# Optimization experiments

Measured on AMD Instinct MI355X. Metric: run time of the kernel, lower is better.

The kernel has to match this reference:

```python
import jax, jax.numpy as jnp
import numpy as np

B, S, H, I, E, TOP_K = 2, 1024, 1024, 2048, 8, 2


def setup_inputs() -> dict:
    key = jax.random.key(0)
    ks = jax.random.split(key, 5)
    return {
        "hidden_states": jax.random.normal(ks[0], (B, S, H), jnp.float32),
        # torch Linear weights are (out, in)
        "router_w": jax.random.normal(ks[1], (E, H), jnp.float32) * 0.02,
        "w1": jax.random.normal(ks[2], (E, I, H), jnp.float32) * 0.02,
        "v": jax.random.normal(ks[3], (E, I, H), jnp.float32) * 0.02,
        "w2": jax.random.normal(ks[4], (E, H, I), jnp.float32) * 0.02,
    }


def _moe(x, router_w, w1, v, w2):
    # x: [T, H] flattened tokens
    T = x.shape[0]
    n_exp = router_w.shape[0]
    logits = x @ router_w.T                                    # [T, E]
    probs = jax.nn.softmax(logits.astype(jnp.float32), axis=-1)
    top_p, top_i = jax.lax.top_k(probs, TOP_K)                 # [T, K]
    top_p = top_p / top_p.sum(axis=-1, keepdims=True)
    top_p = top_p.astype(x.dtype)
    # dense gate matrix [T, E]; zero for unselected experts -> identical math
    # to the torch gather / index_add combine
    gates = jnp.zeros((T, n_exp), x.dtype).at[
        jnp.arange(T)[:, None], top_i].set(top_p)
    out = jnp.zeros_like(x)
    for e in range(n_exp):  # small fixed expert loop keeps peak memory low
        h = jax.nn.gelu(x @ w1[e].T, approximate=False) * (x @ v[e].T)  # [T, I]
        out = out + gates[:, e:e + 1] * (h @ w2[e].T)                   # [T, H]
    return out, logits


def reference(hidden_states, router_w, w1, v, w2):
    b, s, h = hidden_states.shape
    out, logits = _moe(hidden_states.reshape(-1, h), router_w, w1, v, w2)
    return out.reshape(b, s, h), logits
```

## Files before the change

kernel.cpp:

```cpp
#include <hip/hip_runtime.h>
#include <math.h>

#define T 2048
#define HD 1024
#define ID 2048
#define NE 8
#define CSTRIDE 32

typedef short bf16x8 __attribute__((ext_vector_type(8)));
typedef float f32x4 __attribute__((ext_vector_type(4)));
typedef unsigned short u16x4 __attribute__((ext_vector_type(4)));

__device__ __forceinline__ unsigned short f2bf(float f) {
  union { float f; unsigned u; } v; v.f = f;
  unsigned r = v.u + 0x7FFFu + ((v.u >> 16) & 1u);
  return (unsigned short)(r >> 16);
}

__device__ __forceinline__ void cast_chunk16(const float* __restrict__ s,
                                             unsigned short* __restrict__ d,
                                             size_t base) {
  size_t o = base + (size_t)threadIdx.x * 4;
#pragma unroll
  for (int k = 0; k < 4; k++) {
    float4 f = *(const float4*)(s + o + k * 1024);
    u16x4 h;
    h[0] = f2bf(f.x); h[1] = f2bf(f.y); h[2] = f2bf(f.z); h[3] = f2bf(f.w);
    *(u16x4*)(d + o + k * 1024) = h;
  }
}

__device__ __forceinline__ void glds16(const unsigned short* g, unsigned short* l) {
  __builtin_amdgcn_global_load_lds(
      (const __attribute__((address_space(1))) unsigned int*)(g),
      (__attribute__((address_space(3))) unsigned int*)(l), 16, 0, 0);
}

__global__ __launch_bounds__(256) void prep_kernel(
    const float* __restrict__ x, const float* __restrict__ rw,
    const float* __restrict__ w1, const float* __restrict__ v,
    unsigned short* __restrict__ xb, unsigned short* __restrict__ w1b,
    unsigned short* __restrict__ vb, float* __restrict__ logits_out,
    int* __restrict__ pair_rowid, float* __restrict__ pair_gate,
    int* __restrict__ counts) {
  int bx = blockIdx.x;
  if (bx >= 768) {
    int cid = bx - 768;
    const float* s = (cid < 4096) ? w1 : v;
    unsigned short* d = (cid < 4096) ? w1b : vb;
    cast_chunk16(s, d, (size_t)(cid & 4095) * 4096);
    return;
  }
  if (bx >= 256) {
    cast_chunk16(x, xb, (size_t)(bx - 256) * 4096);
    return;
  }
  __shared__ int s_e[16];
  __shared__ int s_rid[16];
  __shared__ float s_gt[16];
  int tid = threadIdx.x;
  int wid = tid >> 6, lane = tid & 63;
  for (int tk = 0; tk < 2; ++tk) {
    int t = bx * 8 + wid * 2 + tk;
    float acc[NE];
#pragma unroll
    for (int e = 0; e < NE; e++) acc[e] = 0.f;
    const float* xrow = x + (size_t)t * HD;
#pragma unroll 2
    for (int j = 0; j < HD; j += 64) {
      float xv = xrow[j + lane];
#pragma unroll
      for (int e = 0; e < NE; e++) acc[e] += xv * rw[e * HD + j + lane];
    }
#pragma unroll
    for (int e = 0; e < NE; e++)
      for (int off = 32; off > 0; off >>= 1) acc[e] += __shfl_xor(acc[e], off, 64);
    if (lane == 0) {
#pragma unroll
      for (int e = 0; e < NE; e++) logits_out[t * NE + e] = acc[e];
      int e0 = 0;
#pragma unroll
      for (int e = 1; e < NE; e++) if (acc[e] > acc[e0]) e0 = e;
      int e1 = (e0 == 0) ? 1 : 0;
#pragma unroll
      for (int e = 0; e < NE; e++)
        if (e != e0 && e != e1 && acc[e] > acc[e1]) e1 = e;
      float b = __expf(acc[e1] - acc[e0]);
      float g0 = 1.f / (1.f + b);
      float g1 = 1.f - g0;
      int slot = (wid * 2 + tk) * 2;
      s_e[slot] = e0; s_rid[slot] = t * 2;     s_gt[slot] = g0;
      s_e[slot + 1] = e1; s_rid[slot + 1] = t * 2 + 1; s_gt[slot + 1] = g1;
    }
  }
  __syncthreads();
  if (tid < NE) {
    int cnt = 0;
#pragma unroll
    for (int k = 0; k < 16; k++) if (s_e[k] == tid) cnt++;
    if (cnt) {
      int base = atomicAdd(&counts[tid * CSTRIDE], cnt);
      int p = 0;
      for (int k = 0; k < 16; k++)
        if (s_e[k] == tid) {
          pair_rowid[tid * T + base + p] = s_rid[k];
          pair_gate[tid * T + base + p] = s_gt[k];
          p++;
        }
    }
  }
}

__global__ __launch_bounds__(256) void gemm1_kernel(
    const unsigned short* __restrict__ xb, const unsigned short* __restrict__ w1b,
    const unsigned short* __restrict__ vb, unsigned short* __restrict__ hb,
    const float* __restrict__ w2, unsigned short* __restrict__ w2b,
    const int* __restrict__ pair_rowid, const int* __restrict__ counts) {
  if (blockIdx.x >= 32) {
    int cid = (blockIdx.x - 32) + 32 * (blockIdx.y + 16 * blockIdx.z);
    cast_chunk16(w2, w2b, (size_t)cid * 4096);
    return;
  }
  int e = blockIdx.z;
  int cnt = counts[e * CSTRIDE];
  int row0 = blockIdx.y * 128;
  if (row0 >= cnt) return;
  __shared__ unsigned short As[128 * 64];
  __shared__ unsigned short B1s[64 * 64];
  __shared__ unsigned short B2s[64 * 64];
  __shared__ int rids[128];
  int tid = threadIdx.x;
  if (tid < 128) {
    int idx = row0 + tid; if (idx > cnt - 1) idx = cnt - 1;
    rids[tid] = pair_rowid[e * T + idx];
  }
  __syncthreads();
  int lane = tid & 63, wid = tid >> 6;
  int wr = wid >> 1, wc = wid & 1;
  int col0 = blockIdx.x * 64;
  int gr = lane >> 3, gc = lane & 7;
  const unsigned short *aA[4], *aB1[2], *aB2[2];
#pragma unroll
  for (int c = 0; c < 4; c++) {
    int row = (c * 4 + wid) * 8 + gr;
    int tok = rids[row] >> 1;
    aA[c] = xb + (size_t)tok * HD + ((gc ^ (row & 7)) * 8);
  }
#pragma unroll
  for (int c = 0; c < 2; c++) {
    int row = (c * 4 + wid) * 8 + gr;
    int kswz = ((gc ^ (row & 7)) * 8);
    aB1[c] = w1b + ((size_t)(e * ID + col0 + row)) * HD + kswz;
    aB2[c] = vb  + ((size_t)(e * ID + col0 + row)) * HD + kswz;
  }
  f32x4 acc1[4][2] = {};
  f32x4 acc3[4][2] = {};
  int mrow = lane & 15, kq = lane >> 4;
  int swzm = mrow & 7;
  for (int kt = 0; kt < HD; kt += 64) {
#pragma unroll
    for (int c = 0; c < 4; c++)
      glds16(aA[c] + kt, &As[(c * 4 + wid) * 512]);
#pragma unroll
    for (int c = 0; c < 2; c++) {
      glds16(aB1[c] + kt, &B1s[(c * 4 + wid) * 512]);
      glds16(aB2[c] + kt, &B2s[(c * 4 + wid) * 512]);
    }
    __syncthreads();
#pragma unroll
    for (int kk = 0; kk < 2; kk++) {
      int g = kk * 4 + kq;
      int ko = ((g ^ swzm) * 8);
      bf16x8 a[4], b1[2], b2[2];
#pragma unroll
      for (int mi = 0; mi < 4; mi++)
        a[mi] = *(const bf16x8*)&As[(wr * 64 + mi * 16 + mrow) * 64 + ko];
#pragma unroll
      for (int ni = 0; ni < 2; ni++) {
        b1[ni] = *(const bf16x8*)&B1s[(wc * 32 + ni * 16 + mrow) * 64 + ko];
        b2[ni] = *(const bf16x8*)&B2s[(wc * 32 + ni * 16 + mrow) * 64 + ko];
      }
#pragma unroll
      for (int mi = 0; mi < 4; mi++)
#pragma unroll
        for (int ni = 0; ni < 2; ni++) {
          acc1[mi][ni] = __builtin_amdgcn_mfma_f32_16x16x32_bf16(a[mi], b1[ni], acc1[mi][ni], 0, 0, 0);
          acc3[mi][ni] = __builtin_amdgcn_mfma_f32_16x16x32_bf16(a[mi], b2[ni], acc3[mi][ni], 0, 0, 0);
        }
    }
    __syncthreads();
  }
  int dcol = lane & 15, drow4 = (lane >> 4) * 4;
#pragma unroll
  for (int mi = 0; mi < 4; mi++)
#pragma unroll
    for (int ni = 0; ni < 2; ni++)
#pragma unroll
      for (int r = 0; r < 4; r++) {
        int lr = wr * 64 + mi * 16 + drow4 + r;
        if (row0 + lr < cnt) {
          float g1v = acc1[mi][ni][r];
          float g3v = acc3[mi][ni][r];
          float hval = 0.5f * g1v * (1.f + erff(g1v * 0.70710678118654752f)) * g3v;
          int rowid = rids[lr];
          hb[(size_t)rowid * ID + col0 + wc * 32 + ni * 16 + dcol] = f2bf(hval);
        }
      }
}

__global__ __launch_bounds__(256) void gemm2_kernel(
    const unsigned short* __restrict__ hb, const unsigned short* __restrict__ w2b,
    float* __restrict__ yb, const int* __restrict__ pair_rowid,
    const float* __restrict__ pair_gate, const int* __restrict__ counts) {
  int e = blockIdx.z;
  int cnt = counts[e * CSTRIDE];
  int row0 = blockIdx.y * 64;
  if (row0 >= cnt) return;
  __shared__ unsigned short As[64 * 64];
  __shared__ unsigned short Bs[64 * 64];
  __shared__ int rids[64];
  __shared__ float gts[64];
  int tid = threadIdx.x;
  if (tid < 64) {
    int idx = row0 + tid; if (idx > cnt - 1) idx = cnt - 1;
    rids[tid] = pair_rowid[e * T + idx];
    gts[tid] = pair_gate[e * T + idx];
  }
  __syncthreads();
  int lane = tid & 63, wid = tid >> 6;
  int wr = wid >> 1, wc = wid & 1;
  int col0 = blockIdx.x * 64;
  int gr = lane >> 3, gc = lane & 7;
  const unsigned short *aA[2], *aB[2];
#pragma unroll
  for (int c = 0; c < 2; c++) {
    int row = (c * 4 + wid) * 8 + gr;
    int kswz = ((gc ^ (row & 7)) * 8);
    aA[c] = hb  + (size_t)rids[row] * ID + kswz;
    aB[c] = w2b + ((size_t)(e * HD + col0 + row)) * ID + kswz;
  }
  f32x4 acc[2][2] = {};
  int mrow = lane & 15, kq = lane >> 4;
  int swzm = mrow & 7;
  for (int kt = 0; kt < ID; kt += 64) {
#pragma unroll
    for (int c = 0; c < 2; c++) {
      glds16(aA[c] + kt, &As[(c * 4 + wid) * 512]);
      glds16(aB[c] + kt, &Bs[(c * 4 + wid) * 512]);
    }
    __syncthreads();
#pragma unroll
    for (int kk = 0; kk < 2; kk++) {
      int g = kk * 4 + kq;
      int ko = ((g ^ swzm) * 8);
      bf16x8 a[2], b[2];
#pragma unroll
      for (int mi = 0; mi < 2; mi++)
        a[mi] = *(const bf16x8*)&As[(wr * 32 + mi * 16 + mrow) * 64 + ko];
#pragma unroll
      for (int ni = 0; ni < 2; ni++)
        b[ni] = *(const bf16x8*)&Bs[(wc * 32 + ni * 16 + mrow) * 64 + ko];
#pragma unroll
      for (int mi = 0; mi < 2; mi++)
#pragma unroll
        for (int ni = 0; ni < 2; ni++)
          acc[mi][ni] = __builtin_amdgcn_mfma_f32_16x16x32_bf16(a[mi], b[ni], acc[mi][ni], 0, 0, 0);
    }
    __syncthreads();
  }
  int dcol = lane & 15, drow4 = (lane >> 4) * 4;
#pragma unroll
  for (int mi = 0; mi < 2; mi++)
#pragma unroll
    for (int ni = 0; ni < 2; ni++)
#pragma unroll
      for (int r = 0; r < 4; r++) {
        int lr = wr * 32 + mi * 16 + drow4 + r;
        if (row0 + lr < cnt) {
          float val = gts[lr] * acc[mi][ni][r];
          yb[(size_t)rids[lr] * HD + col0 + wc * 32 + ni * 16 + dcol] = val;
        }
      }
}

__global__ __launch_bounds__(256) void combine_kernel(
    const float* __restrict__ yb, float* __restrict__ out) {
  size_t t = blockIdx.x;
  int c = threadIdx.x * 4;
  float4 a = *(const float4*)(yb + (t * 2) * HD + c);
  float4 b = *(const float4*)(yb + (t * 2 + 1) * HD + c);
  float4 o;
  o.x = a.x + b.x; o.y = a.y + b.y; o.z = a.z + b.z; o.w = a.w + b.w;
  *(float4*)(out + t * HD + c) = o;
}

extern "C" void kernel_launch(void* const* d_in, const int* in_sizes, int n_in,
                              void* d_out, int out_size, void* d_ws, size_t ws_size,
                              hipStream_t stream) {
  const float* x  = (const float*)d_in[0];
  const float* rw = (const float*)d_in[1];
  const float* w1 = (const float*)d_in[2];
  const float* v  = (const float*)d_in[3];
  const float* w2 = (const float*)d_in[4];
  float* out = (float*)d_out;
  float* logits_out = out + (size_t)T * HD;

  char* ws = (char*)d_ws;
  unsigned short* xb  = (unsigned short*)(ws);
  unsigned short* hb  = (unsigned short*)(ws + (4u << 20));
  unsigned short* w1b = (unsigned short*)(ws + (20u << 20));
  unsigned short* vb  = (unsigned short*)(ws + (52u << 20));
  unsigned short* w2b = (unsigned short*)(ws + (84u << 20));
  float* yb           = (float*)(ws + (20u << 20));
  int*   pair_rowid   = (int*)  (ws + (116u << 20));
  float* pair_gate    = (float*)(ws + (116u << 20) + 65536);
  int*   counts       = (int*)  (ws + (116u << 20) + 131072);

  hipMemsetAsync(counts, 0, NE * CSTRIDE * sizeof(int), stream);

  prep_kernel<<<8960, 256, 0, stream>>>(x, rw, w1, v, xb, w1b, vb,
                                        logits_out, pair_rowid, pair_gate,
                                        counts);
  gemm1_kernel<<<dim3(ID / 64 + 32, T / 128, NE), 256, 0, stream>>>(
      xb, w1b, vb, hb, w2, w2b, pair_rowid, counts);
  gemm2_kernel<<<dim3(HD / 64, T / 64, NE), 256, 0, stream>>>(
      hb, w2b, yb, pair_rowid, pair_gate, counts);
  combine_kernel<<<T, 256, 0, stream>>>(yb, out);
}
```

Before: 327.7 us.

## Fuse fp32-to-bf16 weight casts into double-buffered expert GEMM loads

```diff
diff --git a/kernel.cpp b/kernel.cpp
--- a/kernel.cpp
+++ b/kernel.cpp
@@ -10,11 +10,19 @@
 typedef short bf16x8 __attribute__((ext_vector_type(8)));
 typedef float f32x4 __attribute__((ext_vector_type(4)));
 typedef unsigned short u16x4 __attribute__((ext_vector_type(4)));
+typedef unsigned short u16x8 __attribute__((ext_vector_type(8)));
 
 __device__ __forceinline__ unsigned short f2bf(float f) {
   union { float f; unsigned u; } v; v.f = f;
   unsigned r = v.u + 0x7FFFu + ((v.u >> 16) & 1u);
   return (unsigned short)(r >> 16);
+}
+
+__device__ __forceinline__ u16x8 cvt8(float4 a, float4 b) {
+  u16x8 o;
+  o[0] = f2bf(a.x); o[1] = f2bf(a.y); o[2] = f2bf(a.z); o[3] = f2bf(a.w);
+  o[4] = f2bf(b.x); o[5] = f2bf(b.y); o[6] = f2bf(b.z); o[7] = f2bf(b.w);
+  return o;
 }
 
 __device__ __forceinline__ void cast_chunk16(const float* __restrict__ s,
@@ -38,19 +46,10 @@
 
 __global__ __launch_bounds__(256) void prep_kernel(
     const float* __restrict__ x, const float* __restrict__ rw,
-    const float* __restrict__ w1, const float* __restrict__ v,
-    unsigned short* __restrict__ xb, unsigned short* __restrict__ w1b,
-    unsigned short* __restrict__ vb, float* __restrict__ logits_out,
+    unsigned short* __restrict__ xb, float* __restrict__ logits_out,
     int* __restrict__ pair_rowid, float* __restrict__ pair_gate,
     int* __restrict__ counts) {
   int bx = blockIdx.x;
-  if (bx >= 768) {
-    int cid = bx - 768;
-    const float* s = (cid < 4096) ? w1 : v;
-    unsigned short* d = (cid < 4096) ? w1b : vb;
-    cast_chunk16(s, d, (size_t)(cid & 4095) * 4096);
-    return;
-  }
   if (bx >= 256) {
     cast_chunk16(x, xb, (size_t)(bx - 256) * 4096);
     return;
@@ -112,61 +111,62 @@
 }
 
 __global__ __launch_bounds__(256) void gemm1_kernel(
-    const unsigned short* __restrict__ xb, const unsigned short* __restrict__ w1b,
-    const unsigned short* __restrict__ vb, unsigned short* __restrict__ hb,
-    const float* __restrict__ w2, unsigned short* __restrict__ w2b,
+    const unsigned short* __restrict__ xb, const float* __restrict__ w1,
+    const float* __restrict__ v, unsigned short* __restrict__ hb,
     const int* __restrict__ pair_rowid, const int* __restrict__ counts) {
-  if (blockIdx.x >= 32) {
-    int cid = (blockIdx.x - 32) + 32 * (blockIdx.y + 16 * blockIdx.z);
-    cast_chunk16(w2, w2b, (size_t)cid * 4096);
-    return;
-  }
   int e = blockIdx.z;
   int cnt = counts[e * CSTRIDE];
   int row0 = blockIdx.y * 128;
   if (row0 >= cnt) return;
-  __shared__ unsigned short As[128 * 64];
-  __shared__ unsigned short B1s[64 * 64];
-  __shared__ unsigned short B2s[64 * 64];
-  __shared__ int rids[128];
+  __shared__ unsigned short As[2][128 * 64];
+  __shared__ unsigned short B1s[2][64 * 64];
+  __shared__ unsigned short B2s[2][64 * 64];
   int tid = threadIdx.x;
-  if (tid < 128) {
-    int idx = row0 + tid; if (idx > cnt - 1) idx = cnt - 1;
-    rids[tid] = pair_rowid[e * T + idx];
-  }
-  __syncthreads();
   int lane = tid & 63, wid = tid >> 6;
   int wr = wid >> 1, wc = wid & 1;
   int col0 = blockIdx.x * 64;
   int gr = lane >> 3, gc = lane & 7;
-  const unsigned short *aA[4], *aB1[2], *aB2[2];
+  const unsigned short *aA[4];
+  const float *aB1[2], *aB2[2];
 #pragma unroll
   for (int c = 0; c < 4; c++) {
     int row = (c * 4 + wid) * 8 + gr;
-    int tok = rids[row] >> 1;
+    int idx = row0 + row; if (idx > cnt - 1) idx = cnt - 1;
+    int tok = pair_rowid[e * T + idx] >> 1;
     aA[c] = xb + (size_t)tok * HD + ((gc ^ (row & 7)) * 8);
   }
 #pragma unroll
   for (int c = 0; c < 2; c++) {
     int row = (c * 4 + wid) * 8 + gr;
     int kswz = ((gc ^ (row & 7)) * 8);
-    aB1[c] = w1b + ((size_t)(e * ID + col0 + row)) * HD + kswz;
-    aB2[c] = vb  + ((size_t)(e * ID + col0 + row)) * HD + kswz;
+    aB1[c] = w1 + ((size_t)(e * ID + col0 + row)) * HD + kswz;
+    aB2[c] = v  + ((size_t)(e * ID + col0 + row)) * HD + kswz;
   }
   f32x4 acc1[4][2] = {};
   f32x4 acc3[4][2] = {};
   int mrow = lane & 15, kq = lane >> 4;
   int swzm = mrow & 7;
-  for (int kt = 0; kt < HD; kt += 64) {
-#pragma unroll
-    for (int c = 0; c < 4; c++)
-      glds16(aA[c] + kt, &As[(c * 4 + wid) * 512]);
+  float4 rb1[2][2], rb2[2][2];
+
+  auto issue = [&](int buf, int kt) {
+#pragma unroll
+    for (int c = 0; c < 4; c++) glds16(aA[c] + kt, &As[buf][(c * 4 + wid) * 512]);
 #pragma unroll
     for (int c = 0; c < 2; c++) {
-      glds16(aB1[c] + kt, &B1s[(c * 4 + wid) * 512]);
-      glds16(aB2[c] + kt, &B2s[(c * 4 + wid) * 512]);
-    }
-    __syncthreads();
+      rb1[c][0] = *(const float4*)(aB1[c] + kt);
+      rb1[c][1] = *(const float4*)(aB1[c] + kt + 4);
+      rb2[c][0] = *(const float4*)(aB2[c] + kt);
+      rb2[c][1] = *(const float4*)(aB2[c] + kt + 4);
+    }
+  };
+  auto commitB = [&](int buf) {
+#pragma unroll
+    for (int c = 0; c < 2; c++) {
+      *(u16x8*)&B1s[buf][(c * 4 + wid) * 512 + lane * 8] = cvt8(rb1[c][0], rb1[c][1]);
+      *(u16x8*)&B2s[buf][(c * 4 + wid) * 512 + lane * 8] = cvt8(rb2[c][0], rb2[c][1]);
+    }
+  };
+  auto compute = [&](int buf) {
 #pragma unroll
     for (int kk = 0; kk < 2; kk++) {
       int g = kk * 4 + kq;
@@ -174,11 +174,11 @@
       bf16x8 a[4], b1[2], b2[2];
 #pragma unroll
       for (int mi = 0; mi < 4; mi++)
-        a[mi] = *(const bf16x8*)&As[(wr * 64 + mi * 16 + mrow) * 64 + ko];
+        a[mi] = *(const bf16x8*)&As[buf][(wr * 64 + mi * 16 + mrow) * 64 + ko];
 #pragma unroll
       for (int ni = 0; ni < 2; ni++) {
-        b1[ni] = *(const bf16x8*)&B1s[(wc * 32 + ni * 16 + mrow) * 64 + ko];
-        b2[ni] = *(const bf16x8*)&B2s[(wc * 32 + ni * 16 + mrow) * 64 + ko];
+        b1[ni] = *(const bf16x8*)&B1s[buf][(wc * 32 + ni * 16 + mrow) * 64 + ko];
+        b2[ni] = *(const bf16x8*)&B2s[buf][(wc * 32 + ni * 16 + mrow) * 64 + ko];
       }
 #pragma unroll
       for (int mi = 0; mi < 4; mi++)
@@ -188,8 +188,23 @@
           acc3[mi][ni] = __builtin_amdgcn_mfma_f32_16x16x32_bf16(a[mi], b2[ni], acc3[mi][ni], 0, 0, 0);
         }
     }
+  };
+
+  issue(0, 0);
+  commitB(0);
+  __syncthreads();
+#pragma unroll 1
+  for (int t = 0; t < 16; t += 2) {
+    issue(1, (t + 1) * 64);
+    compute(0);
+    commitB(1);
     __syncthreads();
-  }
+    if (t + 2 < 16) issue(0, (t + 2) * 64);
+    compute(1);
+    if (t + 2 < 16) commitB(0);
+    __syncthreads();
+  }
+
   int dcol = lane & 15, drow4 = (lane >> 4) * 4;
 #pragma unroll
   for (int mi = 0; mi < 4; mi++)
@@ -202,83 +217,106 @@
           float g1v = acc1[mi][ni][r];
           float g3v = acc3[mi][ni][r];
           float hval = 0.5f * g1v * (1.f + erff(g1v * 0.70710678118654752f)) * g3v;
-          int rowid = rids[lr];
+          int rowid = pair_rowid[e * T + row0 + lr];
           hb[(size_t)rowid * ID + col0 + wc * 32 + ni * 16 + dcol] = f2bf(hval);
         }
       }
 }
 
 __global__ __launch_bounds__(256) void gemm2_kernel(
-    const unsigned short* __restrict__ hb, const unsigned short* __restrict__ w2b,
+    const unsigned short* __restrict__ hb, const float* __restrict__ w2,
     float* __restrict__ yb, const int* __restrict__ pair_rowid,
     const float* __restrict__ pair_gate, const int* __restrict__ counts) {
   int e = blockIdx.z;
   int cnt = counts[e * CSTRIDE];
-  int row0 = blockIdx.y * 64;
+  int row0 = blockIdx.y * 128;
   if (row0 >= cnt) return;
-  __shared__ unsigned short As[64 * 64];
-  __shared__ unsigned short Bs[64 * 64];
-  __shared__ int rids[64];
-  __shared__ float gts[64];
+  __shared__ unsigned short As[2][128 * 64];
+  __shared__ unsigned short Bs[2][64 * 64];
   int tid = threadIdx.x;
-  if (tid < 64) {
-    int idx = row0 + tid; if (idx > cnt - 1) idx = cnt - 1;
-    rids[tid] = pair_rowid[e * T + idx];
-    gts[tid] = pair_gate[e * T + idx];
-  }
-  __syncthreads();
   int lane = tid & 63, wid = tid >> 6;
   int wr = wid >> 1, wc = wid & 1;
   int col0 = blockIdx.x * 64;
   int gr = lane >> 3, gc = lane & 7;
-  const unsigned short *aA[2], *aB[2];
+  const unsigned short *aA[4];
+  const float *aB[2];
+#pragma unroll
+  for (int c = 0; c < 4; c++) {
+    int row = (c * 4 + wid) * 8 + gr;
+    int idx = row0 + row; if (idx > cnt - 1) idx = cnt - 1;
+    aA[c] = hb + (size_t)pair_rowid[e * T + idx] * ID + ((gc ^ (row & 7)) * 8);
+  }
 #pragma unroll
   for (int c = 0; c < 2; c++) {
     int row = (c * 4 + wid) * 8 + gr;
     int kswz = ((gc ^ (row & 7)) * 8);
-    aA[c] = hb  + (size_t)rids[row] * ID + kswz;
-    aB[c] = w2b + ((size_t)(e * HD + col0 + row)) * ID + kswz;
-  }
-  f32x4 acc[2][2] = {};
+    aB[c] = w2 + ((size_t)(e * HD + col0 + row)) * ID + kswz;
+  }
+  f32x4 acc[4][2] = {};
   int mrow = lane & 15, kq = lane >> 4;
   int swzm = mrow & 7;
-  for (int kt = 0; kt < ID; kt += 64) {
+  float4 rb[2][2];
+
+  auto issue = [&](int buf, int kt) {
+#pragma unroll
+    for (int c = 0; c < 4; c++) glds16(aA[c] + kt, &As[buf][(c * 4 + wid) * 512]);
 #pragma unroll
     for (int c = 0; c < 2; c++) {
-      glds16(aA[c] + kt, &As[(c * 4 + wid) * 512]);
-      glds16(aB[c] + kt, &Bs[(c * 4 + wid) * 512]);
-    }
-    __syncthreads();
+      rb[c][0] = *(const float4*)(aB[c] + kt);
+      rb[c][1] = *(const float4*)(aB[c] + kt + 4);
+    }
+  };
+  auto commitB = [&](int buf) {
+#pragma unroll
+    for (int c = 0; c < 2; c++)
+      *(u16x8*)&Bs[buf][(c * 4 + wid) * 512 + lane * 8] = cvt8(rb[c][0], rb[c][1]);
+  };
+  auto compute = [&](int buf) {
 #pragma unroll
     for (int kk = 0; kk < 2; kk++) {
       int g = kk * 4 + kq;
       int ko = ((g ^ swzm) * 8);
-      bf16x8 a[2], b[2];
-#pragma unroll
-      for (int mi = 0; mi < 2; mi++)
-        a[mi] = *(const bf16x8*)&As[(wr * 32 + mi * 16 + mrow) * 64 + ko];
+      bf16x8 a[4], b[2];
+#pragma unroll
+      for (int mi = 0; mi < 4; mi++)
+        a[mi] = *(const bf16x8*)&As[buf][(wr * 64 + mi * 16 + mrow) * 64 + ko];
 #pragma unroll
       for (int ni = 0; ni < 2; ni++)
-        b[ni] = *(const bf16x8*)&Bs[(wc * 32 + ni * 16 + mrow) * 64 + ko];
-#pragma unroll
-      for (int mi = 0; mi < 2; mi++)
+        b[ni] = *(const bf16x8*)&Bs[buf][(wc * 32 + ni * 16 + mrow) * 64 + ko];
+#pragma unroll
+      for (int mi = 0; mi < 4; mi++)
 #pragma unroll
         for (int ni = 0; ni < 2; ni++)
           acc[mi][ni] = __builtin_amdgcn_mfma_f32_16x16x32_bf16(a[mi], b[ni], acc[mi][ni], 0, 0, 0);
     }
+  };
+
+  issue(0, 0);
+  commitB(0);
+  __syncthreads();
+#pragma unroll 1
+  for (int t = 0; t < 32; t += 2) {
+    issue(1, (t + 1) * 64);
+    compute(0);
+    commitB(1);
     __syncthreads();
-  }
+    if (t + 2 < 32) issue(0, (t + 2) * 64);
+    compute(1);
+    if (t + 2 < 32) commitB(0);
+    __syncthreads();
+  }
+
   int dcol = lane & 15, drow4 = (lane >> 4) * 4;
 #pragma unroll
-  for (int mi = 0; mi < 2; mi++)
+  for (int mi = 0; mi < 4; mi++)
 #pragma unroll
     for (int ni = 0; ni < 2; ni++)
 #pragma unroll
       for (int r = 0; r < 4; r++) {
-        int lr = wr * 32 + mi * 16 + drow4 + r;
+        int lr = wr * 64 + mi * 16 + drow4 + r;
         if (row0 + lr < cnt) {
-          float val = gts[lr] * acc[mi][ni][r];
-          yb[(size_t)rids[lr] * HD + col0 + wc * 32 + ni * 16 + dcol] = val;
+          float val = pair_gate[e * T + row0 + lr] * acc[mi][ni][r];
+          yb[(size_t)pair_rowid[e * T + row0 + lr] * HD + col0 + wc * 32 + ni * 16 + dcol] = val;
         }
       }
 }
@@ -308,9 +346,6 @@
   char* ws = (char*)d_ws;
   unsigned short* xb  = (unsigned short*)(ws);
   unsigned short* hb  = (unsigned short*)(ws + (4u << 20));
-  unsigned short* w1b = (unsigned short*)(ws + (20u << 20));
-  unsigned short* vb  = (unsigned short*)(ws + (52u << 20));
-  unsigned short* w2b = (unsigned short*)(ws + (84u << 20));
   float* yb           = (float*)(ws + (20u << 20));
   int*   pair_rowid   = (int*)  (ws + (116u << 20));
   float* pair_gate    = (float*)(ws + (116u << 20) + 65536);
@@ -318,12 +353,11 @@
 
   hipMemsetAsync(counts, 0, NE * CSTRIDE * sizeof(int), stream);
 
-  prep_kernel<<<8960, 256, 0, stream>>>(x, rw, w1, v, xb, w1b, vb,
-                                        logits_out, pair_rowid, pair_gate,
-                                        counts);
-  gemm1_kernel<<<dim3(ID / 64 + 32, T / 128, NE), 256, 0, stream>>>(
-      xb, w1b, vb, hb, w2, w2b, pair_rowid, counts);
-  gemm2_kernel<<<dim3(HD / 64, T / 64, NE), 256, 0, stream>>>(
-      hb, w2b, yb, pair_rowid, pair_gate, counts);
+  prep_kernel<<<768, 256, 0, stream>>>(x, rw, xb, logits_out, pair_rowid,
+                                       pair_gate, counts);
+  gemm1_kernel<<<dim3(ID / 64, T / 128, NE), 256, 0, stream>>>(
+      xb, w1, v, hb, pair_rowid, counts);
+  gemm2_kernel<<<dim3(HD / 64, T / 128, NE), 256, 0, stream>>>(
+      hb, w2, yb, pair_rowid, pair_gate, counts);
   combine_kernel<<<T, 256, 0, stream>>>(yb, out);
 }
```

Measured after the change: 349.1 us. 1.07x slower.
